# Performance work log

Hardware: AMD Instinct MI355X
Metric: run time of the kernel (lower is better)

The kernel has to match this reference:

```python
import jax, jax.numpy as jnp
import numpy as np

THRESHOLD = 0.5

def setup_inputs() -> dict:
    key = jax.random.key(0)
    ks = jax.random.split(key, 7)
    dim, hidden = 1024, 4096
    x = jax.random.normal(ks[0], (4, 4096, dim), dtype=jnp.float32)
    # router: Linear(dim, 1)
    W_r = jax.random.normal(ks[1], (dim, 1), dtype=jnp.float32) / np.sqrt(dim)
    b_r = jnp.zeros((1,), dtype=jnp.float32)
    # MLP: Linear(dim, hidden) -> ReLU -> Linear(hidden, dim)
    W1 = jax.random.normal(ks[2], (dim, hidden), dtype=jnp.float32) / np.sqrt(dim)
    b1 = jnp.zeros((hidden,), dtype=jnp.float32)
    W2 = jax.random.normal(ks[3], (hidden, dim), dtype=jnp.float32) / np.sqrt(hidden)
    b2 = jnp.zeros((dim,), dtype=jnp.float32)
    return {"x": x, "W_r": W_r, "b_r": b_r, "W1": W1, "b1": b1, "W2": W2, "b2": b2}

def reference(x, W_r, b_r, W1, b1, W2, b2):
    # router logits per token: [B, S]
    logits = (jnp.einsum('bsd,do->bso', x, W_r) + b_r)[..., 0]
    probs = jax.nn.sigmoid(logits)
    mask = probs > THRESHOLD  # [B, S] bool
    # dense equivalent of gather-MLP-scatter: compute MLP everywhere, select per token
    h = jax.nn.relu(jnp.einsum('bsd,dh->bsh', x, W1) + b1)
    processed = jnp.einsum('bsh,hd->bsd', h, W2) + b2
    output = jnp.where(mask[..., None], processed, x)
    frac = jnp.mean(mask.astype(jnp.float32))
    return (output, frac)
```

## Files before the change

### kernel.cpp

```cpp
#include <hip/hip_runtime.h>
#include <hip/hip_bf16.h>

#define TOKENS 16384
#define DIM 1024
#define HID 4096

typedef __attribute__((ext_vector_type(8))) short short8;
typedef __attribute__((ext_vector_type(4))) float f32x4;

__device__ __forceinline__ unsigned short f2bf(float f) {
  union { float f; unsigned int u; } v; v.f = f;
  unsigned int r = v.u + 0x7fffu + ((v.u >> 16) & 1u);
  return (unsigned short)(r >> 16);
}

__device__ __forceinline__ void async16(const void* g, void* lds) {
  __builtin_amdgcn_global_load_lds((const __attribute__((address_space(1))) void*)g,
                                   (__attribute__((address_space(3))) void*)lds, 16, 0, 0);
}

__global__ __launch_bounds__(256) void router_kernel(
    const float* __restrict__ x, const float* __restrict__ Wr, const float* __restrict__ br,
    float* __restrict__ out, unsigned short* __restrict__ xb,
    int* __restrict__ idx, int* __restrict__ counter)
{
  __shared__ unsigned char selLds[16];
  int wid = threadIdx.x >> 6, lane = threadIdx.x & 63;
  const float4* wr4 = (const float4*)Wr;
  float4 w[4];
#pragma unroll
  for (int j = 0; j < 4; ++j) w[j] = wr4[lane + 64 * j];
  float b0 = br[0];

#pragma unroll
  for (int t = 0; t < 4; ++t) {
    int token = blockIdx.x * 16 + wid * 4 + t;
    const float4* xr = (const float4*)(x + (size_t)token * DIM);
    float4 v[4];
#pragma unroll
    for (int j = 0; j < 4; ++j) v[j] = xr[lane + 64 * j];
    double s = 0.0;
#pragma unroll
    for (int j = 0; j < 4; ++j)
      s += (double)v[j].x * w[j].x + (double)v[j].y * w[j].y +
           (double)v[j].z * w[j].z + (double)v[j].w * w[j].w;
#pragma unroll
    for (int off = 32; off > 0; off >>= 1) s += __shfl_xor(s, off);
    bool sel = ((float)s + b0) > 0.0f;
    if (sel) {
      ushort4* xbr = (ushort4*)(xb + (size_t)token * DIM);
#pragma unroll
      for (int j = 0; j < 4; ++j) {
        ushort4 u;
        u.x = f2bf(v[j].x); u.y = f2bf(v[j].y); u.z = f2bf(v[j].z); u.w = f2bf(v[j].w);
        xbr[lane + 64 * j] = u;
      }
    } else {
      float4* outr = (float4*)(out + (size_t)token * DIM);
#pragma unroll
      for (int j = 0; j < 4; ++j) outr[lane + 64 * j] = v[j];
    }
    if (lane == 0) selLds[wid * 4 + t] = sel ? 1 : 0;
  }
  __syncthreads();
  if (threadIdx.x == 0) {
    int cnt = 0;
#pragma unroll
    for (int i = 0; i < 16; ++i) cnt += selLds[i];
    int p = atomicAdd(counter, cnt);
#pragma unroll
    for (int i = 0; i < 16; ++i)
      if (selLds[i]) idx[p++] = blockIdx.x * 16 + i;
  }
}

__global__ __launch_bounds__(256) void transpose_cast_kernel(
    const float* __restrict__ W, unsigned short* __restrict__ Wt, int R, int C)
{
  __shared__ float tile[32][33];
  int tx = threadIdx.x & 31, ty = threadIdx.x >> 5;
  int c0 = blockIdx.x * 32, r0 = blockIdx.y * 32;
#pragma unroll
  for (int i = 0; i < 32; i += 8)
    tile[ty + i][tx] = W[(size_t)(r0 + ty + i) * C + (c0 + tx)];
  __syncthreads();
#pragma unroll
  for (int i = 0; i < 32; i += 8)
    Wt[(size_t)(c0 + ty + i) * R + (r0 + tx)] = f2bf(tile[tx][ty + i]);
}

__global__ void frac_kernel(const int* __restrict__ counter, float* __restrict__ fr)
{
  fr[0] = (float)(*counter) * (1.0f / (float)TOKENS);
}

template<int N, int K, bool FIRST>
__global__ __launch_bounds__(512, 2) void gemm8_kernel(
    const unsigned short* __restrict__ A, const unsigned short* __restrict__ Bt,
    const float* __restrict__ bias, const int* __restrict__ idxp,
    const int* __restrict__ counter,
    unsigned short* __restrict__ Hout, float* __restrict__ Cout)
{
  constexpr int NT = N / 256;
  constexpr int NKT = K / 64;
  constexpr int NH = NKT * 4;

  int xcd = blockIdx.x & 7, lin = blockIdx.x >> 3;
  int rowb = (lin / NT) * 8 + xcd;
  int colb = lin % NT;

  int cnt = *counter;
  int row0 = rowb * 256;
  if (row0 >= cnt) return;
  int col0 = colb * 256;

  extern __shared__ unsigned short smem[];
  unsigned short* As = smem;
  unsigned short* Bs = smem + 32768;
  int* rowIdxL = (int*)(smem + 65536);

  int tid = threadIdx.x, w = tid >> 6, lane = tid & 63;
  if (tid < 256) rowIdxL[tid] = idxp[row0 + tid];
  __syncthreads();

  int rbase = w * 8 + (lane >> 3);
  int colp  = 8 * ((lane & 7) ^ (lane >> 3));
  const unsigned short* gAp[2][2];
  const unsigned short* gBp[2][2];
#pragma unroll
  for (int hf = 0; hf < 2; ++hf)
#pragma unroll
    for (int L = 0; L < 2; ++L) {
      int r = hf * 128 + L * 64 + rbase;
      int arow = FIRST ? rowIdxL[r] : (row0 + r);
      gAp[hf][L] = A  + (size_t)arow * K + colp;
      gBp[hf][L] = Bt + (size_t)(col0 + r) * K + colp;
    }

  auto stage_half = [&](int n) {
    int T = n >> 2, j = n & 3;
    int half = j >> 1;
    bool isA = (j == 0) || (j == 3);
    unsigned short* base =
        (isA ? As : Bs) + (size_t)((T & 1) * 16384 + half * 8192 + w * 512);
    const unsigned short* s0 = (isA ? gAp[half][0] : gBp[half][0]) + T * 64;
    const unsigned short* s1 = (isA ? gAp[half][1] : gBp[half][1]) + T * 64;
    async16(s0, base);
    async16(s1, base + 4096);
  };

  f32x4 acc[4][4][2];
#pragma unroll
  for (int q = 0; q < 4; ++q)
#pragma unroll
    for (int mi = 0; mi < 4; ++mi)
#pragma unroll
      for (int ni = 0; ni < 2; ++ni) acc[q][mi][ni] = (f32x4){0.f, 0.f, 0.f, 0.f};

  int qr = (w >> 2) * 64, qc = (w & 3) * 32;
  int fr = lane & 15, khalf = lane >> 4;

#pragma unroll
  for (int n = 0; n < 6; ++n) stage_half(n);
  asm volatile("s_waitcnt vmcnt(4)" ::: "memory");
  __builtin_amdgcn_s_barrier();

  for (int t = 0; t < NKT; ++t) {
    int buf = t & 1;
#pragma unroll
    for (int q = 0; q < 4; ++q) {
      const int ah = q >> 1, bh = q & 1;
      unsigned short* Abase = As + (size_t)(buf * 16384 + ah * 8192);
      unsigned short* Bbase = Bs + (size_t)(buf * 16384 + bh * 8192);
      short8 af[4][2], bfr[2][2];
#pragma unroll
      for (int mi = 0; mi < 4; ++mi)
#pragma unroll
        for (int s = 0; s < 2; ++s) {
          int row = qr + mi * 16 + fr;
          af[mi][s] = *(const short8*)&Abase[row * 64 +
                        ((s * 32 + khalf * 8) ^ ((row & 7) << 3))];
        }
#pragma unroll
      for (int ni = 0; ni < 2; ++ni)
#pragma unroll
        for (int s = 0; s < 2; ++s) {
          int row = qc + ni * 16 + fr;
          bfr[ni][s] = *(const short8*)&Bbase[row * 64 +
                        ((s * 32 + khalf * 8) ^ ((row & 7) << 3))];
        }
      int n = t * 4 + q + 6;
      if (n < NH) stage_half(n);
      __builtin_amdgcn_s_barrier();
      asm volatile("s_waitcnt lgkmcnt(0)" ::: "memory");
      __builtin_amdgcn_sched_barrier(0);
      __builtin_amdgcn_s_setprio(1);
#pragma unroll
      for (int mi = 0; mi < 4; ++mi)
#pragma unroll
        for (int ni = 0; ni < 2; ++ni)
#pragma unroll
          for (int s = 0; s < 2; ++s)
            acc[q][mi][ni] = __builtin_amdgcn_mfma_f32_16x16x32_bf16(
                af[mi][s], bfr[ni][s], acc[q][mi][ni], 0, 0, 0);
      __builtin_amdgcn_s_setprio(0);
      __builtin_amdgcn_sched_barrier(0);
      if (q == 3 && t < NKT - 1) {
        if (t < NKT - 2) { asm volatile("s_waitcnt vmcnt(4)" ::: "memory"); }
        else             { asm volatile("s_waitcnt vmcnt(0)" ::: "memory"); }
        __builtin_amdgcn_sched_barrier(0);
      }
      __builtin_amdgcn_s_barrier();
    }
  }

  int cl = lane & 15, rq = lane >> 4;
#pragma unroll
  for (int q = 0; q < 4; ++q) {
    const int ah = q >> 1, bh = q & 1;
#pragma unroll
    for (int mi = 0; mi < 4; ++mi) {
#pragma unroll
      for (int ni = 0; ni < 2; ++ni) {
        int col = col0 + bh * 128 + qc + ni * 16 + cl;
        float bv = bias[col];
#pragma unroll
        for (int r2 = 0; r2 < 4; ++r2) {
          int rloc = ah * 128 + qr + mi * 16 + rq * 4 + r2;
          int grow = row0 + rloc;
          float val = acc[q][mi][ni][r2] + bv;
          if (FIRST) {
            val = val > 0.f ? val : 0.f;
            Hout[(size_t)grow * N + col] = f2bf(val);
          } else if (grow < cnt) {
            int tok = rowIdxL[rloc];
            Cout[(size_t)tok * DIM + col] = val;
          }
        }
      }
    }
  }
}

extern "C" void kernel_launch(void* const* d_in, const int* in_sizes, int n_in,
                              void* d_out, int out_size, void* d_ws, size_t ws_size,
                              hipStream_t stream)
{
  const float* x  = (const float*)d_in[0];
  const float* Wr = (const float*)d_in[1];
  const float* br = (const float*)d_in[2];
  const float* W1 = (const float*)d_in[3];
  const float* b1 = (const float*)d_in[4];
  const float* W2 = (const float*)d_in[5];
  const float* b2 = (const float*)d_in[6];
  float* out = (float*)d_out;

  char* ws = (char*)d_ws;
  int* counter        = (int*)ws;
  int* idx            = (int*)(ws + 256);
  unsigned short* xb  = (unsigned short*)(ws + (1ull  << 20));
  unsigned short* W1T = (unsigned short*)(ws + (34ull << 20));
  unsigned short* W2T = (unsigned short*)(ws + (44ull << 20));
  unsigned short* h   = (unsigned short*)(ws + (54ull << 20));

  constexpr int LDS_BYTES = 132096;
  hipFuncSetAttribute(reinterpret_cast<const void*>(&gemm8_kernel<HID, DIM, true>),
                      hipFuncAttributeMaxDynamicSharedMemorySize, LDS_BYTES);
  hipFuncSetAttribute(reinterpret_cast<const void*>(&gemm8_kernel<DIM, HID, false>),
                      hipFuncAttributeMaxDynamicSharedMemorySize, LDS_BYTES);

  hipMemsetAsync(ws, 0, 256 + TOKENS * 4, stream);

  router_kernel<<<TOKENS / 16, 256, 0, stream>>>(x, Wr, br, out, xb, idx, counter);
  transpose_cast_kernel<<<dim3(HID / 32, DIM / 32), 256, 0, stream>>>(W1, W1T, DIM, HID);
  transpose_cast_kernel<<<dim3(DIM / 32, HID / 32), 256, 0, stream>>>(W2, W2T, HID, DIM);
  frac_kernel<<<1, 1, 0, stream>>>(counter, out + (size_t)TOKENS * DIM);

  gemm8_kernel<HID, DIM, true><<<(HID / 256) * (TOKENS / 256), 512, LDS_BYTES, stream>>>(
      xb, W1T, b1, idx, counter, h, nullptr);
  gemm8_kernel<DIM, HID, false><<<(DIM / 256) * (TOKENS / 256), 512, LDS_BYTES, stream>>>(
      h, W2T, b2, idx, counter, nullptr, out);
}
```

Measured before the change: 396.5 us.

## Add 256x128-tile GEMM for second MLP layer and batch router loads

Replaces the second GEMM (h × W2T, N=1024) with a new kernel that uses 256x128 output tiles, which doubles the number of workgroups so the GPU is better filled when only about half the tokens are selected. The kernel keeps the XCD-aware block mapping, a double-buffered async LDS pipeline and bf16 MFMA. Separately, the router now issues all four tokens' loads up front and interleaves their shuffle reductions to expose memory-level parallelism. Smaller tiles lower per-block arithmetic intensity and re-read A more often, and the batched router loads raise register pressure.

New measurement: 402.4 us. No clear change (+1.5%).

```diff
diff --git a/kernel.cpp b/kernel.cpp
--- a/kernel.cpp
+++ b/kernel.cpp
@@ -31,36 +31,57 @@
 #pragma unroll
   for (int j = 0; j < 4; ++j) w[j] = wr4[lane + 64 * j];
   float b0 = br[0];
-
+  int tok0 = blockIdx.x * 16 + wid * 4;
+
+  float4 v[4][4];
 #pragma unroll
   for (int t = 0; t < 4; ++t) {
-    int token = blockIdx.x * 16 + wid * 4 + t;
-    const float4* xr = (const float4*)(x + (size_t)token * DIM);
-    float4 v[4];
-#pragma unroll
-    for (int j = 0; j < 4; ++j) v[j] = xr[lane + 64 * j];
-    double s = 0.0;
+    const float4* xr = (const float4*)(x + (size_t)(tok0 + t) * DIM);
+#pragma unroll
+    for (int j = 0; j < 4; ++j) v[t][j] = xr[lane + 64 * j];
+  }
+
+  double s[4];
+#pragma unroll
+  for (int t = 0; t < 4; ++t) {
+    double acc = 0.0;
 #pragma unroll
     for (int j = 0; j < 4; ++j)
-      s += (double)v[j].x * w[j].x + (double)v[j].y * w[j].y +
-           (double)v[j].z * w[j].z + (double)v[j].w * w[j].w;
-#pragma unroll
-    for (int off = 32; off > 0; off >>= 1) s += __shfl_xor(s, off);
-    bool sel = ((float)s + b0) > 0.0f;
-    if (sel) {
+      acc += (double)v[t][j].x * w[j].x + (double)v[t][j].y * w[j].y +
+             (double)v[t][j].z * w[j].z + (double)v[t][j].w * w[j].w;
+    s[t] = acc;
+  }
+#pragma unroll
+  for (int off = 32; off > 0; off >>= 1) {
+#pragma unroll
+    for (int t = 0; t < 4; ++t) s[t] += __shfl_xor(s[t], off);
+  }
+
+  bool sel[4];
+#pragma unroll
+  for (int t = 0; t < 4; ++t) sel[t] = ((float)s[t] + b0) > 0.0f;
+
+#pragma unroll
+  for (int t = 0; t < 4; ++t) {
+    int token = tok0 + t;
+    if (sel[t]) {
       ushort4* xbr = (ushort4*)(xb + (size_t)token * DIM);
 #pragma unroll
       for (int j = 0; j < 4; ++j) {
         ushort4 u;
-        u.x = f2bf(v[j].x); u.y = f2bf(v[j].y); u.z = f2bf(v[j].z); u.w = f2bf(v[j].w);
+        u.x = f2bf(v[t][j].x); u.y = f2bf(v[t][j].y);
+        u.z = f2bf(v[t][j].z); u.w = f2bf(v[t][j].w);
         xbr[lane + 64 * j] = u;
       }
     } else {
       float4* outr = (float4*)(out + (size_t)token * DIM);
 #pragma unroll
-      for (int j = 0; j < 4; ++j) outr[lane + 64 * j] = v[j];
-    }
-    if (lane == 0) selLds[wid * 4 + t] = sel ? 1 : 0;
+      for (int j = 0; j < 4; ++j) outr[lane + 64 * j] = v[t][j];
+    }
+  }
+  if (lane == 0) {
+#pragma unroll
+    for (int t = 0; t < 4; ++t) selLds[wid * 4 + t] = sel[t] ? 1 : 0;
   }
   __syncthreads();
   if (threadIdx.x == 0) {
@@ -242,6 +263,146 @@
   }
 }
 
+template<int K>
+__global__ __launch_bounds__(512, 1) void gemm8_n128_kernel(
+    const unsigned short* __restrict__ A, const unsigned short* __restrict__ Bt,
+    const float* __restrict__ bias, const int* __restrict__ idxp,
+    const int* __restrict__ counter, float* __restrict__ Cout)
+{
+  constexpr int NT = DIM / 128;
+  constexpr int NKT = K / 64;
+
+  int xcd = blockIdx.x & 7, lin = blockIdx.x >> 3;
+  int rowb = (lin / NT) * 8 + xcd;
+  int colb = lin % NT;
+
+  int cnt = *counter;
+  int row0 = rowb * 256;
+  if (row0 >= cnt) return;
+  int col0 = colb * 128;
+
+  extern __shared__ unsigned short smem[];
+  unsigned short* As = smem;
+  unsigned short* Bs = smem + 32768;
+  int* rowIdxL = (int*)(smem + 49152);
+
+  int tid = threadIdx.x, w = tid >> 6, lane = tid & 63;
+  if (tid < 256) rowIdxL[tid] = idxp[row0 + tid];
+  __syncthreads();
+
+  int rbase = w * 8 + (lane >> 3);
+  int colp  = 8 * ((lane & 7) ^ (lane >> 3));
+  const unsigned short* gAp[2][2];
+  const unsigned short* gBp[2];
+#pragma unroll
+  for (int hf = 0; hf < 2; ++hf)
+#pragma unroll
+    for (int L = 0; L < 2; ++L)
+      gAp[hf][L] = A + (size_t)(row0 + hf * 128 + L * 64 + rbase) * K + colp;
+#pragma unroll
+  for (int L = 0; L < 2; ++L)
+    gBp[L] = Bt + (size_t)(col0 + L * 64 + rbase) * K + colp;
+
+  auto stageA = [&](int t, int hf) {
+    unsigned short* base = As + (size_t)((t & 1) * 16384 + hf * 8192 + w * 512);
+    async16(gAp[hf][0] + t * 64, base);
+    async16(gAp[hf][1] + t * 64, base + 4096);
+  };
+  auto stageB = [&](int t) {
+    unsigned short* base = Bs + (size_t)((t & 1) * 8192 + w * 512);
+    async16(gBp[0] + t * 64, base);
+    async16(gBp[1] + t * 64, base + 4096);
+  };
+
+  f32x4 acc[2][4][2];
+#pragma unroll
+  for (int q = 0; q < 2; ++q)
+#pragma unroll
+    for (int mi = 0; mi < 4; ++mi)
+#pragma unroll
+      for (int ni = 0; ni < 2; ++ni) acc[q][mi][ni] = (f32x4){0.f, 0.f, 0.f, 0.f};
+
+  int qr = (w >> 2) * 64, qc = (w & 3) * 32;
+  int fr = lane & 15, khalf = lane >> 4;
+
+  stageA(0, 0); stageA(0, 1); stageB(0); stageA(1, 0);
+  asm volatile("s_waitcnt vmcnt(2)" ::: "memory");
+  __builtin_amdgcn_s_barrier();
+
+  for (int t = 0; t < NKT; ++t) {
+    int buf = t & 1;
+#pragma unroll
+    for (int q = 0; q < 2; ++q) {
+      unsigned short* Abase = As + (size_t)(buf * 16384 + q * 8192);
+      unsigned short* Bbase = Bs + (size_t)(buf * 8192);
+      short8 af[4][2], bfr[2][2];
+#pragma unroll
+      for (int mi = 0; mi < 4; ++mi)
+#pragma unroll
+        for (int s = 0; s < 2; ++s) {
+          int row = qr + mi * 16 + fr;
+          af[mi][s] = *(const short8*)&Abase[row * 64 +
+                        ((s * 32 + khalf * 8) ^ ((row & 7) << 3))];
+        }
+#pragma unroll
+      for (int ni = 0; ni < 2; ++ni)
+#pragma unroll
+        for (int s = 0; s < 2; ++s) {
+          int row = qc + ni * 16 + fr;
+          bfr[ni][s] = *(const short8*)&Bbase[row * 64 +
+                        ((s * 32 + khalf * 8) ^ ((row & 7) << 3))];
+        }
+      if (q == 0) {
+        if (t + 1 < NKT) { stageA(t + 1, 1); stageB(t + 1); }
+      } else {
+        if (t + 2 < NKT) { stageA(t + 2, 0); }
+      }
+      __builtin_amdgcn_s_barrier();
+      asm volatile("s_waitcnt lgkmcnt(0)" ::: "memory");
+      __builtin_amdgcn_sched_barrier(0);
+      __builtin_amdgcn_s_setprio(1);
+#pragma unroll
+      for (int mi = 0; mi < 4; ++mi)
+#pragma unroll
+        for (int ni = 0; ni < 2; ++ni)
+#pragma unroll
+          for (int s = 0; s < 2; ++s)
+            acc[q][mi][ni] = __builtin_amdgcn_mfma_f32_16x16x32_bf16(
+                af[mi][s], bfr[ni][s], acc[q][mi][ni], 0, 0, 0);
+      __builtin_amdgcn_s_setprio(0);
+      __builtin_amdgcn_sched_barrier(0);
+      if (q == 1 && t < NKT - 1) {
+        if (t + 2 < NKT) { asm volatile("s_waitcnt vmcnt(2)" ::: "memory"); }
+        else             { asm volatile("s_waitcnt vmcnt(0)" ::: "memory"); }
+        __builtin_amdgcn_sched_barrier(0);
+      }
+      __builtin_amdgcn_s_barrier();
+    }
+  }
+
+  int cl = lane & 15, rq = lane >> 4;
+#pragma unroll
+  for (int q = 0; q < 2; ++q) {
+#pragma unroll
+    for (int mi = 0; mi < 4; ++mi) {
+#pragma unroll
+      for (int ni = 0; ni < 2; ++ni) {
+        int col = col0 + qc + ni * 16 + cl;
+        float bv = bias[col];
+#pragma unroll
+        for (int r2 = 0; r2 < 4; ++r2) {
+          int rloc = q * 128 + qr + mi * 16 + rq * 4 + r2;
+          int grow = row0 + rloc;
+          if (grow < cnt) {
+            int tok = rowIdxL[rloc];
+            Cout[(size_t)tok * DIM + col] = acc[q][mi][ni][r2] + bv;
+          }
+        }
+      }
+    }
+  }
+}
+
 extern "C" void kernel_launch(void* const* d_in, const int* in_sizes, int n_in,
                               void* d_out, int out_size, void* d_ws, size_t ws_size,
                               hipStream_t stream)
@@ -263,11 +424,12 @@
   unsigned short* W2T = (unsigned short*)(ws + (44ull << 20));
   unsigned short* h   = (unsigned short*)(ws + (54ull << 20));
 
-  constexpr int LDS_BYTES = 132096;
+  constexpr int LDS_G1 = 132096;
+  constexpr int LDS_G2 = 99328;
   hipFuncSetAttribute(reinterpret_cast<const void*>(&gemm8_kernel<HID, DIM, true>),
-                      hipFuncAttributeMaxDynamicSharedMemorySize, LDS_BYTES);
-  hipFuncSetAttribute(reinterpret_cast<const void*>(&gemm8_kernel<DIM, HID, false>),
-                      hipFuncAttributeMaxDynamicSharedMemorySize, LDS_BYTES);
+                      hipFuncAttributeMaxDynamicSharedMemorySize, LDS_G1);
+  hipFuncSetAttribute(reinterpret_cast<const void*>(&gemm8_n128_kernel<HID>),
+                      hipFuncAttributeMaxDynamicSharedMemorySize, LDS_G2);
 
   hipMemsetAsync(ws, 0, 256 + TOKENS * 4, stream);
 
@@ -276,8 +438,8 @@
   transpose_cast_kernel<<<dim3(DIM / 32, HID / 32), 256, 0, stream>>>(W2, W2T, HID, DIM);
   frac_kernel<<<1, 1, 0, stream>>>(counter, out + (size_t)TOKENS * DIM);
 
-  gemm8_kernel<HID, DIM, true><<<(HID / 256) * (TOKENS / 256), 512, LDS_BYTES, stream>>>(
+  gemm8_kernel<HID, DIM, true><<<(HID / 256) * (TOKENS / 256), 512, LDS_G1, stream>>>(
       xb, W1T, b1, idx, counter, h, nullptr);
-  gemm8_kernel<DIM, HID, false><<<(DIM / 256) * (TOKENS / 256), 512, LDS_BYTES, stream>>>(
-      h, W2T, b2, idx, counter, nullptr, out);
-}
+  gemm8_n128_kernel<HID><<<(DIM / 128) * (TOKENS / 256), 512, LDS_G2, stream>>>(
+      h, W2T, b2, idx, counter, out);
+}
```
